# Kernel tuning notes

Hardware: AMD Instinct MI355X
Metric: run time of the kernel (lower is better)

Reference implementation:

```python
import jax, jax.numpy as jnp
import numpy as np

D_MODEL = 1024
NUM_HEADS = 8
D_K = D_MODEL // NUM_HEADS


def setup_inputs() -> dict:
    key = jax.random.key(0)
    ks = jax.random.split(key, 11)
    B, S, D = 2, 2048, D_MODEL
    scale = 1.0 / np.sqrt(D)
    return {
        "Q": jax.random.normal(ks[0], (B, S, D), jnp.float32),
        "K": jax.random.normal(ks[1], (B, S, D), jnp.float32),
        "V": jax.random.normal(ks[2], (B, S, D), jnp.float32),
        # torch nn.Linear weights are stored (out_features, in_features)
        "Wq": jax.random.normal(ks[3], (D, D), jnp.float32) * scale,
        "bq": jnp.zeros((D,), jnp.float32),
        "Wk": jax.random.normal(ks[4], (D, D), jnp.float32) * scale,
        "bk": jnp.zeros((D,), jnp.float32),
        "Wv": jax.random.normal(ks[5], (D, D), jnp.float32) * scale,
        "bv": jnp.zeros((D,), jnp.float32),
        "Wo": jax.random.normal(ks[6], (D, D), jnp.float32) * scale,
        "bo": jnp.zeros((D,), jnp.float32),
    }


def reference(Q, K, V, Wq, bq, Wk, bk, Wv, bv, Wo, bo):
    B, S, D = Q.shape
    H, dk = NUM_HEADS, D_K
    # projections (torch Linear: x @ W.T + b), then split heads -> [B,H,S,dk]
    q = (Q @ Wq.T + bq).reshape(B, S, H, dk).transpose(0, 2, 1, 3)
    k = (K @ Wk.T + bk).reshape(B, S, H, dk).transpose(0, 2, 1, 3)
    v = (V @ Wv.T + bv).reshape(B, S, H, dk).transpose(0, 2, 1, 3)
    scores = jnp.einsum("bhqd,bhkd->bhqk", q, k) / jnp.sqrt(jnp.float32(dk))
    attn = jax.nn.softmax(scores, axis=-1)  # [B,H,S,S]
    ctx = jnp.einsum("bhqk,bhkd->bhqd", attn, v)
    concat = ctx.transpose(0, 2, 1, 3).reshape(B, S, D)
    out = concat @ Wo.T + bo
    return out, attn
```

## Files before the change

kernel.cpp:

```cpp
#include <hip/hip_runtime.h>

#define S_LEN 2048
#define DMODEL 1024
#define NHEADS 8
#define DK 128
#define BATCH 2

typedef _Float16 h16;
typedef __attribute__((ext_vector_type(8))) _Float16 half8v;
typedef __attribute__((ext_vector_type(4))) float float4v;

#define GLD16(gp, lp)                                                  \
  __builtin_amdgcn_global_load_lds(                                    \
      (const __attribute__((address_space(1))) void*)(gp),             \
      (__attribute__((address_space(3))) void*)(lp), 16, 0, 0)

__global__ __launch_bounds__(256) void cvt_kernel(const float* __restrict__ src,
                                                  h16* __restrict__ dst, int n8) {
  int i = blockIdx.x * 256 + threadIdx.x;
  if (i < n8) {
    const float4* s = (const float4*)src + (size_t)i * 2;
    float4 a = s[0], b = s[1];
    half8v h = {(h16)a.x, (h16)a.y, (h16)a.z, (h16)a.w,
                (h16)b.x, (h16)b.y, (h16)b.z, (h16)b.w};
    *((half8v*)dst + i) = h;
  }
}

__global__ __launch_bounds__(256) void qkv_gemm(
    const h16* __restrict__ qf, const h16* __restrict__ kf, const h16* __restrict__ vf,
    const h16* __restrict__ wq, const h16* __restrict__ wk, const h16* __restrict__ wv,
    const float* __restrict__ bq, const float* __restrict__ bk, const float* __restrict__ bv,
    h16* __restrict__ qh, h16* __restrict__ kh, h16* __restrict__ vt) {
  __shared__ h16 As[128 * 32];
  __shared__ h16 Bs[128 * 32];

  const int z = blockIdx.z;
  const h16* A = z == 0 ? qf : (z == 1 ? kf : vf);
  const h16* Bw = z == 0 ? wq : (z == 1 ? wk : wv);
  const float* bias = z == 0 ? bq : (z == 1 ? bk : bv);
  h16* outp = z == 0 ? qh : (z == 1 ? kh : vt);

  const int t = threadIdx.x, lane = t & 63, w = t >> 6;
  const int m0 = blockIdx.y * 128, n0 = blockIdx.x * 128;
  const int wm = (w >> 1) * 64, wn = (w & 1) * 64;
  const int lcol = lane & 15, lquad = lane >> 4;

  float4v acc[4][4];
  for (int i = 0; i < 4; ++i)
    for (int j = 0; j < 4; ++j) acc[i][j] = {0.f, 0.f, 0.f, 0.f};

  for (int kt = 0; kt < 1024; kt += 32) {
    __syncthreads();
    for (int j = 0; j < 2; ++j) {
      int i = w * 2 + j;
      int row = i * 16 + (lane >> 2);
      int c4 = (lane & 3) ^ ((row >> 1) & 3);
      GLD16(A + (size_t)(m0 + row) * 1024 + kt + c4 * 8, As + i * 512);
      GLD16(Bw + (size_t)(n0 + row) * 1024 + kt + c4 * 8, Bs + i * 512);
    }
    __syncthreads();

    half8v af[4], bf[4];
    for (int mi = 0; mi < 4; ++mi) {
      int r = wm + mi * 16 + lcol;
      af[mi] = *(const half8v*)(As + r * 32 + ((lquad ^ ((r >> 1) & 3)) << 3));
    }
    for (int ni = 0; ni < 4; ++ni) {
      int r = wn + ni * 16 + lcol;
      bf[ni] = *(const half8v*)(Bs + r * 32 + ((lquad ^ ((r >> 1) & 3)) << 3));
    }
    for (int mi = 0; mi < 4; ++mi)
      for (int ni = 0; ni < 4; ++ni)
        acc[mi][ni] = __builtin_amdgcn_mfma_f32_16x16x32_f16(af[mi], bf[ni],
                                                             acc[mi][ni], 0, 0, 0);
  }

  for (int ni = 0; ni < 4; ++ni) {
    int gn = n0 + wn + ni * 16 + lcol;
    float bv = bias[gn];
    int hh = gn >> 7, dv = gn & 127;
    for (int mi = 0; mi < 4; ++mi) {
      int gmb = m0 + wm + mi * 16 + lquad * 4;
      for (int r = 0; r < 4; ++r) {
        int gm = gmb + r;
        float v = acc[mi][ni][r] + bv;
        int b = gm >> 11, s = gm & 2047;
        if (z < 2)
          outp[((size_t)(b * NHEADS + hh) * S_LEN + s) * DK + dv] = (h16)v;
        else
          outp[((size_t)(b * NHEADS + hh) * DK + dv) * S_LEN + s] = (h16)v;
      }
    }
  }
}

__global__ __launch_bounds__(256) void out_gemm(const h16* __restrict__ A,
                                                const h16* __restrict__ Bw,
                                                const float* __restrict__ bias,
                                                float* __restrict__ C) {
  __shared__ h16 As[64 * 32];
  __shared__ h16 Bs[128 * 32];

  const int t = threadIdx.x, lane = t & 63, w = t >> 6;
  const int m0 = blockIdx.y * 64, n0 = blockIdx.x * 128;
  const int wm = (w >> 1) * 32, wn = (w & 1) * 64;
  const int lcol = lane & 15, lquad = lane >> 4;

  float4v acc[2][4];
  for (int i = 0; i < 2; ++i)
    for (int j = 0; j < 4; ++j) acc[i][j] = {0.f, 0.f, 0.f, 0.f};

  for (int kt = 0; kt < 1024; kt += 32) {
    __syncthreads();
    {
      int i = w;
      int row = i * 16 + (lane >> 2);
      int c4 = (lane & 3) ^ ((row >> 1) & 3);
      GLD16(A + (size_t)(m0 + row) * 1024 + kt + c4 * 8, As + i * 512);
    }
    for (int j = 0; j < 2; ++j) {
      int i = w * 2 + j;
      int row = i * 16 + (lane >> 2);
      int c4 = (lane & 3) ^ ((row >> 1) & 3);
      GLD16(Bw + (size_t)(n0 + row) * 1024 + kt + c4 * 8, Bs + i * 512);
    }
    __syncthreads();

    half8v af[2], bf[4];
    for (int mi = 0; mi < 2; ++mi) {
      int r = wm + mi * 16 + lcol;
      af[mi] = *(const half8v*)(As + r * 32 + ((lquad ^ ((r >> 1) & 3)) << 3));
    }
    for (int ni = 0; ni < 4; ++ni) {
      int r = wn + ni * 16 + lcol;
      bf[ni] = *(const half8v*)(Bs + r * 32 + ((lquad ^ ((r >> 1) & 3)) << 3));
    }
    for (int mi = 0; mi < 2; ++mi)
      for (int ni = 0; ni < 4; ++ni)
        acc[mi][ni] = __builtin_amdgcn_mfma_f32_16x16x32_f16(af[mi], bf[ni],
                                                             acc[mi][ni], 0, 0, 0);
  }

  for (int ni = 0; ni < 4; ++ni) {
    int gn = n0 + wn + ni * 16 + lcol;
    float bv = bias[gn];
    for (int mi = 0; mi < 2; ++mi) {
      int gmb = m0 + wm + mi * 16 + lquad * 4;
      for (int r = 0; r < 4; ++r)
        C[(size_t)(gmb + r) * 1024 + gn] = acc[mi][ni][r] + bv;
    }
  }
}

__device__ inline void attn_bid(int& bh, int& q0) {
  int id = blockIdx.y * 32 + blockIdx.x;
  int xcd = id & 7, rank = id >> 3;
  bh = xcd + 8 * (rank >> 5);
  q0 = (rank & 31) * 64;
}

__global__ __launch_bounds__(256) void lsum_kernel(const h16* __restrict__ qh,
                                                   const h16* __restrict__ kh,
                                                   float* __restrict__ linv) {
  __shared__ h16 Qs[64 * 128];
  __shared__ h16 Ks[64 * 128];

  const int t = threadIdx.x, lane = t & 63, w = t >> 6;
  const int lcol = lane & 15, lquad = lane >> 4;
  int bh, q0;
  attn_bid(bh, q0);
  const float scale = 0.08838834764831845f;

  for (int j = 0; j < 4; ++j) {
    int i = w * 4 + j;
    int row = i * 4 + (lane >> 4);
    int c4 = (lane & 15) ^ (row & 7);
    GLD16(qh + ((size_t)bh * S_LEN + q0 + row) * DK + c4 * 8, Qs + i * 512);
  }
  __syncthreads();
  half8v aq[4];
  {
    int r = 16 * w + lcol;
    for (int ks = 0; ks < 4; ++ks)
      aq[ks] = *(const half8v*)(Qs + r * 128 + (((ks * 4 + lquad) ^ (r & 7)) << 3));
  }

  float lsum[4] = {0.f, 0.f, 0.f, 0.f};

  for (int kt = 0; kt < 32; ++kt) {
    __syncthreads();
    for (int j = 0; j < 4; ++j) {
      int i = w * 4 + j;
      int row = i * 4 + (lane >> 4);
      int c4 = (lane & 15) ^ (row & 7);
      GLD16(kh + ((size_t)bh * S_LEN + kt * 64 + row) * DK + c4 * 8, Ks + i * 512);
    }
    __syncthreads();

    for (int ni = 0; ni < 4; ++ni) {
      float4v sacc = {0.f, 0.f, 0.f, 0.f};
      int r = ni * 16 + lcol;
      for (int ks = 0; ks < 4; ++ks) {
        half8v bk = *(const half8v*)(Ks + r * 128 + (((ks * 4 + lquad) ^ (r & 7)) << 3));
        sacc = __builtin_amdgcn_mfma_f32_16x16x32_f16(aq[ks], bk, sacc, 0, 0, 0);
      }
      for (int rr = 0; rr < 4; ++rr) lsum[rr] += __expf(sacc[rr] * scale);
    }
  }

  for (int rr = 0; rr < 4; ++rr) {
    float v = lsum[rr];
    for (int off = 1; off < 16; off <<= 1) v += __shfl_xor(v, off);
    if (lcol == 0)
      linv[(size_t)bh * S_LEN + q0 + 16 * w + lquad * 4 + rr] = 1.f / v;
  }
}

__global__ __launch_bounds__(256) void attn_kernel(const h16* __restrict__ qh,
                                                   const h16* __restrict__ kh,
                                                   const h16* __restrict__ vt,
                                                   const float* __restrict__ linv,
                                                   float* __restrict__ attn,
                                                   h16* __restrict__ ctxb) {
  __shared__ h16 Qs[64 * 128];
  __shared__ h16 Ks[64 * 128];
  __shared__ h16 Vts[128 * 64];
  __shared__ h16 Ps[4][16 * 72];

  const int t = threadIdx.x, lane = t & 63, w = t >> 6;
  const int lcol = lane & 15, lquad = lane >> 4;
  int bh, q0;
  attn_bid(bh, q0);
  const int b = bh >> 3, h = bh & 7;
  const float scale = 0.08838834764831845f;

  for (int j = 0; j < 4; ++j) {
    int i = w * 4 + j;
    int row = i * 4 + (lane >> 4);
    int c4 = (lane & 15) ^ (row & 7);
    GLD16(qh + ((size_t)bh * S_LEN + q0 + row) * DK + c4 * 8, Qs + i * 512);
  }
  __syncthreads();
  half8v aq[4];
  {
    int r = 16 * w + lcol;
    for (int ks = 0; ks < 4; ++ks)
      aq[ks] = *(const half8v*)(Qs + r * 128 + (((ks * 4 + lquad) ^ (r & 7)) << 3));
  }
  float il[4];
  for (int rr = 0; rr < 4; ++rr)
    il[rr] = linv[(size_t)bh * S_LEN + q0 + 16 * w + lquad * 4 + rr];

  float4v cacc[8];
  for (int i = 0; i < 8; ++i) cacc[i] = {0.f, 0.f, 0.f, 0.f};

  float* abase = attn + ((size_t)bh * S_LEN + q0 + 16 * w) * S_LEN;
  h16* Psw = &Ps[w][0];

  for (int kt = 0; kt < 32; ++kt) {
    __syncthreads();
    for (int j = 0; j < 4; ++j) {
      int i = w * 4 + j;
      int row = i * 4 + (lane >> 4);
      int c4 = (lane & 15) ^ (row & 7);
      GLD16(kh + ((size_t)bh * S_LEN + kt * 64 + row) * DK + c4 * 8, Ks + i * 512);
    }
    for (int j = 0; j < 4; ++j) {
      int i = w * 4 + j;
      int row = i * 8 + (lane >> 3);
      int c4 = (lane & 7) ^ (row & 7);
      GLD16(vt + ((size_t)bh * DK + row) * S_LEN + kt * 64 + c4 * 8, Vts + i * 512);
    }
    __syncthreads();

    float4v sacc[4];
    for (int ni = 0; ni < 4; ++ni) {
      sacc[ni] = {0.f, 0.f, 0.f, 0.f};
      int r = ni * 16 + lcol;
      for (int ks = 0; ks < 4; ++ks) {
        half8v bk = *(const half8v*)(Ks + r * 128 + (((ks * 4 + lquad) ^ (r & 7)) << 3));
        sacc[ni] = __builtin_amdgcn_mfma_f32_16x16x32_f16(aq[ks], bk, sacc[ni], 0, 0, 0);
      }
    }

    for (int ni = 0; ni < 4; ++ni)
      for (int rr = 0; rr < 4; ++rr) {
        float p = __expf(sacc[ni][rr] * scale) * il[rr];
        abase[(size_t)(lquad * 4 + rr) * S_LEN + kt * 64 + ni * 16 + lcol] = p;
        Psw[(lquad * 4 + rr) * 72 + ni * 16 + lcol] = (h16)p;
      }

    half8v ap[2];
    for (int k2 = 0; k2 < 2; ++k2)
      ap[k2] = *(const half8v*)(Psw + lcol * 72 + k2 * 32 + lquad * 8);
    for (int n2 = 0; n2 < 8; ++n2) {
      int r = n2 * 16 + lcol;
      for (int k2 = 0; k2 < 2; ++k2) {
        half8v bv = *(const half8v*)(Vts + r * 64 + (((k2 * 4 + lquad) ^ (r & 7)) << 3));
        cacc[n2] = __builtin_amdgcn_mfma_f32_16x16x32_f16(ap[k2], bv, cacc[n2], 0, 0, 0);
      }
    }
  }

  h16* cb = ctxb + ((size_t)b * S_LEN + q0 + 16 * w) * DMODEL + h * DK;
  for (int n2 = 0; n2 < 8; ++n2)
    for (int rr = 0; rr < 4; ++rr)
      cb[(size_t)(lquad * 4 + rr) * DMODEL + n2 * 16 + lcol] = (h16)cacc[n2][rr];
}

extern "C" void kernel_launch(void* const* d_in, const int* in_sizes, int n_in,
                              void* d_out, int out_size, void* d_ws, size_t ws_size,
                              hipStream_t stream) {
  const float* Q  = (const float*)d_in[0];
  const float* K  = (const float*)d_in[1];
  const float* V  = (const float*)d_in[2];
  const float* Wq = (const float*)d_in[3];
  const float* bq = (const float*)d_in[4];
  const float* Wk = (const float*)d_in[5];
  const float* bk = (const float*)d_in[6];
  const float* Wv = (const float*)d_in[7];
  const float* bv = (const float*)d_in[8];
  const float* Wo = (const float*)d_in[9];
  const float* bo = (const float*)d_in[10];

  float* out  = (float*)d_out;
  float* attn = out + (size_t)BATCH * S_LEN * DMODEL;

  const size_t NTOK = (size_t)BATCH * S_LEN * DMODEL;
  const size_t NW = (size_t)DMODEL * DMODEL;
  h16* qf  = (h16*)d_ws;
  h16* kf  = qf + NTOK;
  h16* vf  = kf + NTOK;
  h16* wqh = vf + NTOK;
  h16* wkh = wqh + NW;
  h16* wvh = wkh + NW;
  h16* woh = wvh + NW;
  h16* qh  = woh + NW;
  h16* kh  = qh + NTOK;
  h16* vt  = kh + NTOK;
  h16* ctxb = qf;
  float* linv = (float*)kf;

  dim3 gb(256);
  cvt_kernel<<<dim3(NTOK / 8 / 256), gb, 0, stream>>>(Q, qf, NTOK / 8);
  cvt_kernel<<<dim3(NTOK / 8 / 256), gb, 0, stream>>>(K, kf, NTOK / 8);
  cvt_kernel<<<dim3(NTOK / 8 / 256), gb, 0, stream>>>(V, vf, NTOK / 8);
  cvt_kernel<<<dim3(NW / 8 / 256), gb, 0, stream>>>(Wq, wqh, NW / 8);
  cvt_kernel<<<dim3(NW / 8 / 256), gb, 0, stream>>>(Wk, wkh, NW / 8);
  cvt_kernel<<<dim3(NW / 8 / 256), gb, 0, stream>>>(Wv, wvh, NW / 8);
  cvt_kernel<<<dim3(NW / 8 / 256), gb, 0, stream>>>(Wo, woh, NW / 8);

  qkv_gemm<<<dim3(8, 32, 3), gb, 0, stream>>>(qf, kf, vf, wqh, wkh, wvh,
                                              bq, bk, bv, qh, kh, vt);
  lsum_kernel<<<dim3(32, 16), gb, 0, stream>>>(qh, kh, linv);
  attn_kernel<<<dim3(32, 16), gb, 0, stream>>>(qh, kh, vt, linv, attn, ctxb);
  out_gemm<<<dim3(8, 64), gb, 0, stream>>>(ctxb, woh, bo, out);
}
```

Measured before the change: 494.5 us.

## Fuse row-sum and attention kernels with double-buffered PV pipeline, merge conversions

Merges the seven fp32-to-fp16 conversion launches into one kernel. Folds the separate softmax-denominator kernel into the attention kernel as a first pass over K, with the four per-wave partial sums combined through LDS. The attention work is also redistributed so each wave handles all 64 query rows against 16 keys and a 32-column slice of the context. V and P tiles are double-buffered so the P·V step for the previous tile overlaps the next tile's loads and QK. This adds register pressure (launch_bounds 256,2 and larger per-thread fragments) and changes the attn store pattern to per-wave key columns.

```diff
diff --git a/kernel.cpp b/kernel.cpp
--- a/kernel.cpp
+++ b/kernel.cpp
@@ -15,16 +15,34 @@
       (const __attribute__((address_space(1))) void*)(gp),             \
       (__attribute__((address_space(3))) void*)(lp), 16, 0, 0)
 
-__global__ __launch_bounds__(256) void cvt_kernel(const float* __restrict__ src,
-                                                  h16* __restrict__ dst, int n8) {
+__global__ __launch_bounds__(256) void cvt_all(
+    const float* __restrict__ q, const float* __restrict__ k, const float* __restrict__ v,
+    const float* __restrict__ wq, const float* __restrict__ wk, const float* __restrict__ wv,
+    const float* __restrict__ wo,
+    h16* __restrict__ dq, h16* __restrict__ dk, h16* __restrict__ dv,
+    h16* __restrict__ dwq, h16* __restrict__ dwk, h16* __restrict__ dwv,
+    h16* __restrict__ dwo) {
   int i = blockIdx.x * 256 + threadIdx.x;
-  if (i < n8) {
-    const float4* s = (const float4*)src + (size_t)i * 2;
-    float4 a = s[0], b = s[1];
-    half8v h = {(h16)a.x, (h16)a.y, (h16)a.z, (h16)a.w,
-                (h16)b.x, (h16)b.y, (h16)b.z, (h16)b.w};
-    *((half8v*)dst + i) = h;
-  }
+  const float* src;
+  h16* dst;
+  int off;
+  if (i < 1572864) {
+    int seg = i >> 19;
+    off = i & 524287;
+    src = seg == 0 ? q : (seg == 1 ? k : v);
+    dst = seg == 0 ? dq : (seg == 1 ? dk : dv);
+  } else {
+    int j = i - 1572864;
+    int seg = j >> 17;
+    off = j & 131071;
+    src = seg == 0 ? wq : (seg == 1 ? wk : (seg == 2 ? wv : wo));
+    dst = seg == 0 ? dwq : (seg == 1 ? dwk : (seg == 2 ? dwv : dwo));
+  }
+  const float4* s = (const float4*)src + (size_t)off * 2;
+  float4 a = s[0], b = s[1];
+  half8v h = {(h16)a.x, (h16)a.y, (h16)a.z, (h16)a.w,
+              (h16)b.x, (h16)b.y, (h16)b.z, (h16)b.w};
+  *((half8v*)dst + off) = h;
 }
 
 __global__ __launch_bounds__(256) void qkv_gemm(
@@ -78,13 +96,13 @@
 
   for (int ni = 0; ni < 4; ++ni) {
     int gn = n0 + wn + ni * 16 + lcol;
-    float bv = bias[gn];
+    float bvv = bias[gn];
     int hh = gn >> 7, dv = gn & 127;
     for (int mi = 0; mi < 4; ++mi) {
       int gmb = m0 + wm + mi * 16 + lquad * 4;
       for (int r = 0; r < 4; ++r) {
         int gm = gmb + r;
-        float v = acc[mi][ni][r] + bv;
+        float v = acc[mi][ni][r] + bvv;
         int b = gm >> 11, s = gm & 2047;
         if (z < 2)
           outp[((size_t)(b * NHEADS + hh) * S_LEN + s) * DK + dv] = (h16)v;
@@ -144,11 +162,11 @@
 
   for (int ni = 0; ni < 4; ++ni) {
     int gn = n0 + wn + ni * 16 + lcol;
-    float bv = bias[gn];
+    float bvv = bias[gn];
     for (int mi = 0; mi < 2; ++mi) {
       int gmb = m0 + wm + mi * 16 + lquad * 4;
       for (int r = 0; r < 4; ++r)
-        C[(size_t)(gmb + r) * 1024 + gn] = acc[mi][ni][r] + bv;
+        C[(size_t)(gmb + r) * 1024 + gn] = acc[mi][ni][r] + bvv;
     }
   }
 }
@@ -160,73 +178,32 @@
   q0 = (rank & 31) * 64;
 }
 
-__global__ __launch_bounds__(256) void lsum_kernel(const h16* __restrict__ qh,
-                                                   const h16* __restrict__ kh,
-                                                   float* __restrict__ linv) {
-  __shared__ h16 Qs[64 * 128];
+#define PV_STEP(PP, VV)                                                        \
+  {                                                                            \
+    half8v ap[4][2];                                                           \
+    for (int mi = 0; mi < 4; ++mi)                                             \
+      for (int k2 = 0; k2 < 2; ++k2)                                           \
+        ap[mi][k2] =                                                           \
+            *(const half8v*)((PP) + (mi * 16 + lcol) * 72 + k2 * 32 + lquad * 8); \
+    for (int nd = 0; nd < 2; ++nd) {                                           \
+      int r = w * 32 + nd * 16 + lcol;                                         \
+      for (int k2 = 0; k2 < 2; ++k2) {                                         \
+        half8v bv = *(const half8v*)((VV) + r * 64 +                           \
+                                     (((k2 * 4 + lquad) ^ (r & 7)) << 3));     \
+        for (int mi = 0; mi < 4; ++mi)                                         \
+          cacc[mi][nd] = __builtin_amdgcn_mfma_f32_16x16x32_f16(               \
+              ap[mi][k2], bv, cacc[mi][nd], 0, 0, 0);                          \
+      }                                                                        \
+    }                                                                          \
+  }
+
+__global__ __launch_bounds__(256, 2) void attn_fused(
+    const h16* __restrict__ qh, const h16* __restrict__ kh,
+    const h16* __restrict__ vt, float* __restrict__ attn,
+    h16* __restrict__ ctxb) {
   __shared__ h16 Ks[64 * 128];
-
-  const int t = threadIdx.x, lane = t & 63, w = t >> 6;
-  const int lcol = lane & 15, lquad = lane >> 4;
-  int bh, q0;
-  attn_bid(bh, q0);
-  const float scale = 0.08838834764831845f;
-
-  for (int j = 0; j < 4; ++j) {
-    int i = w * 4 + j;
-    int row = i * 4 + (lane >> 4);
-    int c4 = (lane & 15) ^ (row & 7);
-    GLD16(qh + ((size_t)bh * S_LEN + q0 + row) * DK + c4 * 8, Qs + i * 512);
-  }
-  __syncthreads();
-  half8v aq[4];
-  {
-    int r = 16 * w + lcol;
-    for (int ks = 0; ks < 4; ++ks)
-      aq[ks] = *(const half8v*)(Qs + r * 128 + (((ks * 4 + lquad) ^ (r & 7)) << 3));
-  }
-
-  float lsum[4] = {0.f, 0.f, 0.f, 0.f};
-
-  for (int kt = 0; kt < 32; ++kt) {
-    __syncthreads();
-    for (int j = 0; j < 4; ++j) {
-      int i = w * 4 + j;
-      int row = i * 4 + (lane >> 4);
-      int c4 = (lane & 15) ^ (row & 7);
-      GLD16(kh + ((size_t)bh * S_LEN + kt * 64 + row) * DK + c4 * 8, Ks + i * 512);
-    }
-    __syncthreads();
-
-    for (int ni = 0; ni < 4; ++ni) {
-      float4v sacc = {0.f, 0.f, 0.f, 0.f};
-      int r = ni * 16 + lcol;
-      for (int ks = 0; ks < 4; ++ks) {
-        half8v bk = *(const half8v*)(Ks + r * 128 + (((ks * 4 + lquad) ^ (r & 7)) << 3));
-        sacc = __builtin_amdgcn_mfma_f32_16x16x32_f16(aq[ks], bk, sacc, 0, 0, 0);
-      }
-      for (int rr = 0; rr < 4; ++rr) lsum[rr] += __expf(sacc[rr] * scale);
-    }
-  }
-
-  for (int rr = 0; rr < 4; ++rr) {
-    float v = lsum[rr];
-    for (int off = 1; off < 16; off <<= 1) v += __shfl_xor(v, off);
-    if (lcol == 0)
-      linv[(size_t)bh * S_LEN + q0 + 16 * w + lquad * 4 + rr] = 1.f / v;
-  }
-}
-
-__global__ __launch_bounds__(256) void attn_kernel(const h16* __restrict__ qh,
-                                                   const h16* __restrict__ kh,
-                                                   const h16* __restrict__ vt,
-                                                   const float* __restrict__ linv,
-                                                   float* __restrict__ attn,
-                                                   h16* __restrict__ ctxb) {
-  __shared__ h16 Qs[64 * 128];
-  __shared__ h16 Ks[64 * 128];
-  __shared__ h16 Vts[128 * 64];
-  __shared__ h16 Ps[4][16 * 72];
+  __shared__ h16 Vts[2][128 * 64];
+  __shared__ h16 Ps[2][64 * 72];
 
   const int t = threadIdx.x, lane = t & 63, w = t >> 6;
   const int lcol = lane & 15, lquad = lane >> 4;
@@ -239,24 +216,19 @@
     int i = w * 4 + j;
     int row = i * 4 + (lane >> 4);
     int c4 = (lane & 15) ^ (row & 7);
-    GLD16(qh + ((size_t)bh * S_LEN + q0 + row) * DK + c4 * 8, Qs + i * 512);
+    GLD16(qh + ((size_t)bh * S_LEN + q0 + row) * DK + c4 * 8, Ks + i * 512);
   }
   __syncthreads();
-  half8v aq[4];
-  {
-    int r = 16 * w + lcol;
+  half8v aq[4][4];
+  for (int mi = 0; mi < 4; ++mi) {
+    int r = mi * 16 + lcol;
     for (int ks = 0; ks < 4; ++ks)
-      aq[ks] = *(const half8v*)(Qs + r * 128 + (((ks * 4 + lquad) ^ (r & 7)) << 3));
-  }
-  float il[4];
-  for (int rr = 0; rr < 4; ++rr)
-    il[rr] = linv[(size_t)bh * S_LEN + q0 + 16 * w + lquad * 4 + rr];
-
-  float4v cacc[8];
-  for (int i = 0; i < 8; ++i) cacc[i] = {0.f, 0.f, 0.f, 0.f};
-
-  float* abase = attn + ((size_t)bh * S_LEN + q0 + 16 * w) * S_LEN;
-  h16* Psw = &Ps[w][0];
+      aq[mi][ks] = *(const half8v*)(Ks + r * 128 + (((ks * 4 + lquad) ^ (r & 7)) << 3));
+  }
+
+  float ls[4][4];
+  for (int mi = 0; mi < 4; ++mi)
+    for (int rr = 0; rr < 4; ++rr) ls[mi][rr] = 0.f;
 
   for (int kt = 0; kt < 32; ++kt) {
     __syncthreads();
@@ -266,47 +238,97 @@
       int c4 = (lane & 15) ^ (row & 7);
       GLD16(kh + ((size_t)bh * S_LEN + kt * 64 + row) * DK + c4 * 8, Ks + i * 512);
     }
+    __syncthreads();
+
+    float4v sacc[4];
+    for (int mi = 0; mi < 4; ++mi) sacc[mi] = {0.f, 0.f, 0.f, 0.f};
+    int r = w * 16 + lcol;
+    for (int ks = 0; ks < 4; ++ks) {
+      half8v bk = *(const half8v*)(Ks + r * 128 + (((ks * 4 + lquad) ^ (r & 7)) << 3));
+      for (int mi = 0; mi < 4; ++mi)
+        sacc[mi] = __builtin_amdgcn_mfma_f32_16x16x32_f16(aq[mi][ks], bk, sacc[mi], 0, 0, 0);
+    }
+    for (int mi = 0; mi < 4; ++mi)
+      for (int rr = 0; rr < 4; ++rr) ls[mi][rr] += __expf(sacc[mi][rr] * scale);
+  }
+
+  float* red = (float*)Ps[0];
+  for (int mi = 0; mi < 4; ++mi)
+    for (int rr = 0; rr < 4; ++rr) {
+      float vsum = ls[mi][rr];
+      for (int off = 1; off < 16; off <<= 1) vsum += __shfl_xor(vsum, off);
+      if (lcol == 0) red[w * 64 + mi * 16 + lquad * 4 + rr] = vsum;
+    }
+  __syncthreads();
+  float il[4][4];
+  for (int mi = 0; mi < 4; ++mi)
+    for (int rr = 0; rr < 4; ++rr) {
+      int row = mi * 16 + lquad * 4 + rr;
+      il[mi][rr] = 1.f / (red[row] + red[64 + row] + red[128 + row] + red[192 + row]);
+    }
+
+  float4v cacc[4][2];
+  for (int mi = 0; mi < 4; ++mi)
+    for (int nd = 0; nd < 2; ++nd) cacc[mi][nd] = {0.f, 0.f, 0.f, 0.f};
+
+  float* abase = attn + ((size_t)bh * S_LEN + q0 + lquad * 4) * S_LEN + w * 16 + lcol;
+
+  for (int kt = 0; kt < 32; ++kt) {
+    int p = kt & 1;
+    __syncthreads();
+    for (int j = 0; j < 4; ++j) {
+      int i = w * 4 + j;
+      int row = i * 4 + (lane >> 4);
+      int c4 = (lane & 15) ^ (row & 7);
+      GLD16(kh + ((size_t)bh * S_LEN + kt * 64 + row) * DK + c4 * 8, Ks + i * 512);
+    }
     for (int j = 0; j < 4; ++j) {
       int i = w * 4 + j;
       int row = i * 8 + (lane >> 3);
       int c4 = (lane & 7) ^ (row & 7);
-      GLD16(vt + ((size_t)bh * DK + row) * S_LEN + kt * 64 + c4 * 8, Vts + i * 512);
-    }
-    __syncthreads();
+      GLD16(vt + ((size_t)bh * DK + row) * S_LEN + kt * 64 + c4 * 8, Vts[p] + i * 512);
+    }
+    __syncthreads();
+
+    if (kt > 0) {
+      const h16* Psr = Ps[p ^ 1];
+      const h16* Vr = Vts[p ^ 1];
+      PV_STEP(Psr, Vr);
+    }
 
     float4v sacc[4];
-    for (int ni = 0; ni < 4; ++ni) {
-      sacc[ni] = {0.f, 0.f, 0.f, 0.f};
-      int r = ni * 16 + lcol;
+    for (int mi = 0; mi < 4; ++mi) sacc[mi] = {0.f, 0.f, 0.f, 0.f};
+    {
+      int r = w * 16 + lcol;
       for (int ks = 0; ks < 4; ++ks) {
         half8v bk = *(const half8v*)(Ks + r * 128 + (((ks * 4 + lquad) ^ (r & 7)) << 3));
-        sacc[ni] = __builtin_amdgcn_mfma_f32_16x16x32_f16(aq[ks], bk, sacc[ni], 0, 0, 0);
+        for (int mi = 0; mi < 4; ++mi)
+          sacc[mi] = __builtin_amdgcn_mfma_f32_16x16x32_f16(aq[mi][ks], bk, sacc[mi], 0, 0, 0);
       }
     }
 
-    for (int ni = 0; ni < 4; ++ni)
+    h16* Psw = Ps[p] + lquad * 4 * 72 + w * 16 + lcol;
+    float* ab = abase + (size_t)kt * 64;
+    for (int mi = 0; mi < 4; ++mi)
       for (int rr = 0; rr < 4; ++rr) {
-        float p = __expf(sacc[ni][rr] * scale) * il[rr];
-        abase[(size_t)(lquad * 4 + rr) * S_LEN + kt * 64 + ni * 16 + lcol] = p;
-        Psw[(lquad * 4 + rr) * 72 + ni * 16 + lcol] = (h16)p;
+        float pv = __expf(sacc[mi][rr] * scale) * il[mi][rr];
+        ab[(size_t)(mi * 16 + rr) * S_LEN] = pv;
+        Psw[(mi * 16 + rr) * 72] = (h16)pv;
       }
-
-    half8v ap[2];
-    for (int k2 = 0; k2 < 2; ++k2)
-      ap[k2] = *(const half8v*)(Psw + lcol * 72 + k2 * 32 + lquad * 8);
-    for (int n2 = 0; n2 < 8; ++n2) {
-      int r = n2 * 16 + lcol;
-      for (int k2 = 0; k2 < 2; ++k2) {
-        half8v bv = *(const half8v*)(Vts + r * 64 + (((k2 * 4 + lquad) ^ (r & 7)) << 3));
-        cacc[n2] = __builtin_amdgcn_mfma_f32_16x16x32_f16(ap[k2], bv, cacc[n2], 0, 0, 0);
-      }
-    }
-  }
-
-  h16* cb = ctxb + ((size_t)b * S_LEN + q0 + 16 * w) * DMODEL + h * DK;
-  for (int n2 = 0; n2 < 8; ++n2)
-    for (int rr = 0; rr < 4; ++rr)
-      cb[(size_t)(lquad * 4 + rr) * DMODEL + n2 * 16 + lcol] = (h16)cacc[n2][rr];
+  }
+
+  __syncthreads();
+  {
+    const h16* Psr = Ps[1];
+    const h16* Vr = Vts[1];
+    PV_STEP(Psr, Vr);
+  }
+
+  h16* cb = ctxb + ((size_t)b * S_LEN + q0 + lquad * 4) * DMODEL + h * DK + w * 32;
+  for (int mi = 0; mi < 4; ++mi)
+    for (int nd = 0; nd < 2; ++nd)
+      for (int rr = 0; rr < 4; ++rr)
+        cb[(size_t)(mi * 16 + rr) * DMODEL + nd * 16 + lcol] = (h16)cacc[mi][nd][rr];
 }
 
 extern "C" void kernel_launch(void* const* d_in, const int* in_sizes, int n_in,
@@ -340,20 +362,12 @@
   h16* kh  = qh + NTOK;
   h16* vt  = kh + NTOK;
   h16* ctxb = qf;
-  float* linv = (float*)kf;
 
   dim3 gb(256);
-  cvt_kernel<<<dim3(NTOK / 8 / 256), gb, 0, stream>>>(Q, qf, NTOK / 8);
-  cvt_kernel<<<dim3(NTOK / 8 / 256), gb, 0, stream>>>(K, kf, NTOK / 8);
-  cvt_kernel<<<dim3(NTOK / 8 / 256), gb, 0, stream>>>(V, vf, NTOK / 8);
-  cvt_kernel<<<dim3(NW / 8 / 256), gb, 0, stream>>>(Wq, wqh, NW / 8);
-  cvt_kernel<<<dim3(NW / 8 / 256), gb, 0, stream>>>(Wk, wkh, NW / 8);
-  cvt_kernel<<<dim3(NW / 8 / 256), gb, 0, stream>>>(Wv, wvh, NW / 8);
-  cvt_kernel<<<dim3(NW / 8 / 256), gb, 0, stream>>>(Wo, woh, NW / 8);
-
+  cvt_all<<<dim3(8192), gb, 0, stream>>>(Q, K, V, Wq, Wk, Wv, Wo,
+                                         qf, kf, vf, wqh, wkh, wvh, woh);
   qkv_gemm<<<dim3(8, 32, 3), gb, 0, stream>>>(qf, kf, vf, wqh, wkh, wvh,
                                               bq, bk, bv, qh, kh, vt);
-  lsum_kernel<<<dim3(32, 16), gb, 0, stream>>>(qh, kh, linv);
-  attn_kernel<<<dim3(32, 16), gb, 0, stream>>>(qh, kh, vt, linv, attn, ctxb);
+  attn_fused<<<dim3(32, 16), gb, 0, stream>>>(qh, kh, vt, attn, ctxb);
   out_gemm<<<dim3(8, 64), gb, 0, stream>>>(ctxb, woh, bo, out);
 }
```

Result: faster. 471.7 us (-4.6%).
